# Performance work log

Measured on AMD Instinct MI355X. Metric: run time of the kernel, lower is better.

## Reference

```python
import jax, jax.numpy as jnp
import numpy as np

B, S, E, P, H, F = 4, 4096, 256, 32, 8, 1024
DH = E // H
LN_EPS = 1e-5


def setup_inputs() -> dict:
    key = jax.random.key(0)
    ks = jax.random.split(key, 12)
    dt = jnp.float32
    return {
        "src": jax.random.normal(ks[0], (B, S, E), dt),
        "pos_embed": jax.random.normal(ks[1], (B, P, S), dt),
        # learnable positional transform (pos_linear: P -> P)
        "Wpos": jax.random.normal(ks[2], (P, P), dt) * (1.0 / np.sqrt(P)),
        "bpos": jnp.zeros((P,), dt),
        # RBF kernel hyperparameters (ScaleKernel(RBFKernel)) -- positive scalars
        "lengthscale": jnp.full((), 2.0, dt),
        "outputscale": jnp.full((), 1.0, dt),
        # value / output projections of multihead attention
        "Wv": jax.random.normal(ks[3], (E, E), dt) * (1.0 / np.sqrt(E)),
        "bv": jnp.zeros((E,), dt),
        "Wo": jax.random.normal(ks[4], (E, E), dt) * (1.0 / np.sqrt(E)),
        "bo": jnp.zeros((E,), dt),
        # feed-forward
        "W1": jax.random.normal(ks[5], (F, E), dt) * (1.0 / np.sqrt(E)),
        "b1": jnp.zeros((F,), dt),
        "W2": jax.random.normal(ks[6], (E, F), dt) * (1.0 / np.sqrt(F)),
        "b2": jnp.zeros((E,), dt),
        # layer norms
        "ln1_g": jnp.ones((E,), dt), "ln1_b": jnp.zeros((E,), dt),
        "ln2_g": jnp.ones((E,), dt), "ln2_b": jnp.zeros((E,), dt),
    }


def _layer_norm(x, g, b):
    mu = jnp.mean(x, -1, keepdims=True)
    var = jnp.mean(jnp.square(x - mu), -1, keepdims=True)
    return (x - mu) * jax.lax.rsqrt(var + LN_EPS) * g + b


def _rbf_scores(x, lengthscale, outputscale):
    # x: [B, S, P] -> scaled RBF kernel matrix [B, S, S]
    xs = x / lengthscale
    sq = jnp.sum(xs * xs, axis=-1)  # [B, S]
    d2 = sq[:, :, None] + sq[:, None, :] - 2.0 * jnp.einsum('bsp,btp->bst', xs, xs)
    d2 = jnp.maximum(d2, 0.0)
    return outputscale * jnp.exp(-0.5 * d2)


def reference(src, pos_embed, Wpos, bpos, lengthscale, outputscale,
              Wv, bv, Wo, bo, W1, b1, W2, b2, ln1_g, ln1_b, ln2_g, ln2_b):
    b, s, e = src.shape
    # learnable positional transform: [B,P,S] -> [B,S,P] -> linear -> back
    pe = jnp.einsum('bps,op->bos', pos_embed, Wpos) + bpos[None, :, None]  # [B,P,S]
    # GP-kernel attention scores over sequence positions
    scores = _rbf_scores(pe.transpose(0, 2, 1), lengthscale, outputscale)  # [B,S,S]
    attn = jax.nn.softmax(scores, axis=-1)
    # value projection, per-head weighted sum (scores shared across heads)
    v = (src @ Wv.T + bv).reshape(b, s, H, DH)
    ctx = jnp.einsum('bqk,bkhd->bqhd', attn, v).reshape(b, s, e)
    attn_out = ctx @ Wo.T + bo
    x = _layer_norm(src + attn_out, ln1_g, ln1_b)
    ff = jax.nn.relu(x @ W1.T + b1) @ W2.T + b2
    return _layer_norm(x + ff, ln2_g, ln2_b)
```

## Files before the change

### kernel.cpp

```cpp
#include <hip/hip_runtime.h>
#include <stdint.h>

#define BN 4
#define SN 4096
#define EN 256
#define PN 32
#define FN 1024
#define BS (BN*SN)
#define PAUG 64

typedef uint16_t bf16_t;
typedef short v4s  __attribute__((ext_vector_type(4)));
typedef short v8s  __attribute__((ext_vector_type(8)));
typedef __bf16 bf16x8 __attribute__((ext_vector_type(8)));
typedef float v4f   __attribute__((ext_vector_type(4)));
typedef float v16f  __attribute__((ext_vector_type(16)));

#define MFMA16(a,b,c) __builtin_amdgcn_mfma_f32_16x16x32_bf16(a,b,c,0,0,0)
#define MFMA32(a,b,c) __builtin_amdgcn_mfma_f32_32x32x16_bf16(a,b,c,0,0,0)

__device__ __forceinline__ float b2f(bf16_t x){
    uint32_t u = ((uint32_t)x) << 16; float f; __builtin_memcpy(&f, &u, 4); return f;
}
__device__ __forceinline__ bf16_t f2b(float f){
    uint32_t u; __builtin_memcpy(&u, &f, 4);
    u += 0x7FFFu + ((u >> 16) & 1u);
    return (bf16_t)(u >> 16);
}
__device__ __forceinline__ bf16x8 ldb8(const bf16_t* p){
    v8s r = *(const v8s*)p; return __builtin_bit_cast(bf16x8, r);
}
__device__ __forceinline__ bf16x8 ldb8u(const bf16_t* p){
    v4s lo = *(const v4s*)p;
    v4s hi = *(const v4s*)(p + 4);
    v8s r = __builtin_shufflevector(lo, hi, 0,1,2,3,4,5,6,7);
    return __builtin_bit_cast(bf16x8, r);
}
__device__ __forceinline__ float ldsc(const float* p){ return *p; }
__device__ __forceinline__ float ldsc(const bf16_t* p){ return b2f(*p); }
__device__ __forceinline__ void stsc(float* p, float v){ *p = v; }
__device__ __forceinline__ void stsc(bf16_t* p, float v){ *p = f2b(v); }

#if __has_builtin(__builtin_amdgcn_exp2f)
__device__ __forceinline__ float fexp2(float x){ return __builtin_amdgcn_exp2f(x); }
#else
__device__ __forceinline__ float fexp2(float x){ return exp2f(x); }
#endif

#if __has_builtin(__builtin_amdgcn_cvt_pk_bf16_f32)
typedef __bf16 bf16x2 __attribute__((ext_vector_type(2)));
__device__ __forceinline__ uint32_t pkbf16(float a, float b){
    bf16x2 r = __builtin_amdgcn_cvt_pk_bf16_f32(a, b);
    return __builtin_bit_cast(uint32_t, r);
}
#else
__device__ __forceinline__ uint32_t pkbf16(float a, float b){
    return (uint32_t)f2b(a) | ((uint32_t)f2b(b) << 16);
}
#endif

typedef const __attribute__((address_space(1))) uint32_t* glds_gp;
typedef __attribute__((address_space(3))) uint32_t* glds_lp;
__device__ __forceinline__ void glds16(const bf16_t* g, bf16_t* l){
    __builtin_amdgcn_global_load_lds((glds_gp)g, (glds_lp)l, 16, 0, 0);
}

__global__ __launch_bounds__(256) void prep_kernel(
    const float* __restrict__ src, bf16_t* __restrict__ srcb,
    const float* __restrict__ Wv, bf16_t* __restrict__ Wvb,
    const float* __restrict__ Wo, bf16_t* __restrict__ Wob,
    const float* __restrict__ W1, bf16_t* __restrict__ W1b,
    const float* __restrict__ W2, bf16_t* __restrict__ W2b,
    const float* __restrict__ pos, const float* __restrict__ Wp,
    const float* __restrict__ bp,  const float* __restrict__ lsp,
    bf16_t* __restrict__ xk, bf16_t* __restrict__ xq)
{
    __shared__ float Wsh[PN*PN];
    __shared__ float bsh[PN];
    int bid = blockIdx.x;
    int tid = threadIdx.x;

    if (bid < 4736){
        const float* sp; bf16_t* dp; int off;
        if (bid < 4096){ sp = src; dp = srcb; off = (bid*256 + tid)*4; }
        else {
            int i = ((bid - 4096)*256 + tid)*4;
            if      (i <  65536){ sp=Wv; dp=Wvb; off=i; }
            else if (i < 131072){ sp=Wo; dp=Wob; off=i- 65536; }
            else if (i < 393216){ sp=W1; dp=W1b; off=i-131072; }
            else                { sp=W2; dp=W2b; off=i-393216; }
        }
        float4 f = *(const float4*)(sp + off);
        v4s o;
        o.x = (short)f2b(f.x); o.y = (short)f2b(f.y);
        o.z = (short)f2b(f.z); o.w = (short)f2b(f.w);
        *(v4s*)(dp + off) = o;
        return;
    }

    int pb = bid - 4736;
    int b  = pb >> 4;
    int s  = (pb & 15)*256 + tid;

    for (int i = tid; i < PN*PN; i += 256) Wsh[i] = Wp[i];
    if (tid < PN) bsh[tid] = bp[tid];
    __syncthreads();

    float inv_ls = 1.0f / lsp[0];
    const float c1f = 1.4426950408889634f;

    float col[PN];
    #pragma unroll
    for (int p = 0; p < PN; p++) col[p] = pos[((size_t)b*PN + p)*SN + s];

    uint16_t xb[PN], qb[PN];
    float sq = 0.f;
    #pragma unroll 4
    for (int o = 0; o < PN; o++){
        float pe = bsh[o];
        #pragma unroll
        for (int p = 0; p < PN; p++) pe += col[p] * Wsh[o*PN + p];
        float pv = pe * inv_ls;
        uint16_t h = f2b(pv);
        xb[o] = h;
        qb[o] = f2b(c1f * pv);
        float xr = b2f(h);
        sq += xr * xr;
    }

    size_t base = ((size_t)b*SN + s) * PAUG;
    v8s pk[8];
    #pragma unroll
    for (int c = 0; c < 4; c++)
        #pragma unroll
        for (int j = 0; j < 8; j++) ((short*)&pk[c])[j] = (short)xb[c*8 + j];
    #pragma unroll
    for (int c = 4; c < 8; c++)
        #pragma unroll
        for (int j = 0; j < 8; j++) ((short*)&pk[c])[j] = 0;
    ((short*)&pk[4])[0] = (short)f2b(-0.5f * sq);
    ((short*)&pk[4])[1] = (short)0x3F80;
    #pragma unroll
    for (int c = 0; c < 8; c++) *(v8s*)(xk + base + c*8) = pk[c];

    #pragma unroll
    for (int c = 0; c < 4; c++)
        #pragma unroll
        for (int j = 0; j < 8; j++) ((short*)&pk[c])[j] = (short)qb[c*8 + j];
    ((short*)&pk[4])[0] = (short)f2b(c1f);
    ((short*)&pk[4])[1] = (short)f2b(-0.5f * sq * c1f);
    #pragma unroll
    for (int c = 0; c < 8; c++) *(v8s*)(xq + base + c*8) = pk[c];
}

template<int EPI, typename OutT>
__global__ __launch_bounds__(256) void gemm_t(
    const bf16_t* __restrict__ A, const bf16_t* __restrict__ W,
    const float* __restrict__ bias, OutT* __restrict__ out,
    bf16_t* __restrict__ vt, int N, int K)
{
    __shared__ __align__(16) bf16_t At[2][4096];
    __shared__ __align__(16) bf16_t Wt[2][4096];
    int tid = threadIdx.x;
    int lane = tid & 63, wv = tid >> 6, col = lane & 15, quad = lane >> 4;
    int m0 = blockIdx.x * 64, n0 = blockIdx.y * 64;
    int nck = K >> 6;

    int srow = tid >> 3;
    int spc  = (tid & 7) ^ (srow & 7);
    const bf16_t* asrc = A + (size_t)(m0 + srow)*K + spc*8;
    const bf16_t* wsrc = W + (size_t)(n0 + srow)*K + spc*8;

    v4f acc[4];
    #pragma unroll
    for (int t = 0; t < 4; t++) acc[t] = (v4f){0.f,0.f,0.f,0.f};

    glds16(asrc, &At[0][tid*8]);
    glds16(asrc + (size_t)32*K, &At[0][2048 + tid*8]);
    glds16(wsrc, &Wt[0][tid*8]);
    glds16(wsrc + (size_t)32*K, &Wt[0][2048 + tid*8]);
    __syncthreads();

    for (int c = 0; c < nck; c++){
        int cb = c & 1;
        if (c + 1 < nck){
            glds16(asrc + (c+1)*64, &At[cb^1][tid*8]);
            glds16(asrc + (size_t)32*K + (c+1)*64, &At[cb^1][2048 + tid*8]);
            glds16(wsrc + (c+1)*64, &Wt[cb^1][tid*8]);
            glds16(wsrc + (size_t)32*K + (c+1)*64, &Wt[cb^1][2048 + tid*8]);
        }
        #pragma unroll
        for (int kc = 0; kc < 2; kc++){
            int pc = ((kc*4 + quad) ^ (col & 7)) * 8;
            bf16x8 a = ldb8(&At[cb][(wv*16 + col)*64 + pc]);
            #pragma unroll
            for (int t = 0; t < 4; t++){
                bf16x8 b = ldb8(&Wt[cb][(t*16 + col)*64 + pc]);
                acc[t] = MFMA16(a, b, acc[t]);
            }
        }
        __syncthreads();
    }

    float bfv[4];
    #pragma unroll
    for (int t = 0; t < 4; t++) bfv[t] = bias[n0 + t*16 + col];

    if constexpr (EPI == 3){
        __shared__ uint16_t Tsh[64*74];
        #pragma unroll
        for (int r = 0; r < 4; r++)
            #pragma unroll
            for (int t = 0; t < 4; t++)
                Tsh[(wv*16 + quad*4 + r)*74 + t*16 + col] = f2b(acc[t][r] + bfv[t]);
        __syncthreads();
        int e = tid >> 2, sc = tid & 3;
        int b = m0 >> 12;
        int sbat = m0 & (SN-1);
        int eb   = (n0 + e) >> 5;
        int l31e = (n0 + e) & 31;
        int k16  = (sbat >> 4) + sc;
        v8s p0, p1;
        #pragma unroll
        for (int i = 0; i < 8; i++) ((short*)&p0)[i] = (short)Tsh[(sc*16 + i)*74 + e];
        #pragma unroll
        for (int i = 0; i < 8; i++) ((short*)&p1)[i] = (short)Tsh[(sc*16 + 8 + i)*74 + e];
        bf16_t* dst = vt + ((((size_t)b*8 + eb)*256 + k16)*64 + l31e)*8;
        *(v8s*)dst = p0;
        *(v8s*)(dst + 256) = p1;
    } else {
        #pragma unroll
        for (int r = 0; r < 4; r++){
            int row = m0 + wv*16 + quad*4 + r;
            #pragma unroll
            for (int t = 0; t < 4; t++){
                float y = acc[t][r] + bfv[t];
                if constexpr (EPI == 1) y = fmaxf(y, 0.f);
                stsc(out + (size_t)row*N + n0 + t*16 + col, y);
            }
        }
    }
}

template<int EPI>
__global__ __launch_bounds__(256, 2) void gemm128(
    const bf16_t* __restrict__ A, const bf16_t* __restrict__ W,
    const float* __restrict__ bias, bf16_t* __restrict__ out,
    int N, int K)
{
    __shared__ __align__(16) bf16_t At[2][8192];
    __shared__ __align__(16) bf16_t Wt[2][8192];
    int tid = threadIdx.x;
    int lane = tid & 63, wv = tid >> 6, col = lane & 15, quad = lane >> 4;
    int m0 = blockIdx.x * 128, n0 = blockIdx.y * 128;
    int nck = K >> 6;

    int srow = tid >> 3;
    int spc  = (tid & 7) ^ (srow & 7);
    const bf16_t* asrc = A + (size_t)(m0 + srow)*K + spc*8;
    const bf16_t* wsrc = W + (size_t)(n0 + srow)*K + spc*8;

    v4f acc[2][8];
    #pragma unroll
    for (int mi = 0; mi < 2; mi++)
        #pragma unroll
        for (int t = 0; t < 8; t++) acc[mi][t] = (v4f){0.f,0.f,0.f,0.f};

    #pragma unroll
    for (int s = 0; s < 4; s++){
        glds16(asrc + (size_t)(s*32)*K, &At[0][s*2048 + tid*8]);
        glds16(wsrc + (size_t)(s*32)*K, &Wt[0][s*2048 + tid*8]);
    }
    __syncthreads();

    for (int c = 0; c < nck; c++){
        int cb = c & 1;
        if (c + 1 < nck){
            #pragma unroll
            for (int s = 0; s < 4; s++){
                glds16(asrc + (size_t)(s*32)*K + (c+1)*64, &At[cb^1][s*2048 + tid*8]);
                glds16(wsrc + (size_t)(s*32)*K + (c+1)*64, &Wt[cb^1][s*2048 + tid*8]);
            }
        }
        #pragma unroll
        for (int kc = 0; kc < 2; kc++){
            int pc = ((kc*4 + quad) ^ (col & 7)) * 8;
            bf16x8 a[2];
            #pragma unroll
            for (int mi = 0; mi < 2; mi++)
                a[mi] = ldb8(&At[cb][(wv*32 + mi*16 + col)*64 + pc]);
            #pragma unroll
            for (int t = 0; t < 8; t++){
                bf16x8 b = ldb8(&Wt[cb][(t*16 + col)*64 + pc]);
                #pragma unroll
                for (int mi = 0; mi < 2; mi++)
                    acc[mi][t] = MFMA16(a[mi], b, acc[mi][t]);
            }
        }
        __syncthreads();
    }

    float bfv[8];
    #pragma unroll
    for (int t = 0; t < 8; t++) bfv[t] = bias[n0 + t*16 + col];

    #pragma unroll
    for (int mi = 0; mi < 2; mi++){
        #pragma unroll
        for (int r = 0; r < 4; r++){
            int row = m0 + wv*32 + mi*16 + quad*4 + r;
            #pragma unroll
            for (int t = 0; t < 8; t++){
                float y = acc[mi][t][r] + bfv[t];
                if constexpr (EPI == 1) y = fmaxf(y, 0.f);
                out[(size_t)row*N + n0 + t*16 + col] = f2b(y);
            }
        }
    }
}

template<typename OutT, typename ResT>
__global__ __launch_bounds__(256) void ln_kernel(
    const bf16_t* __restrict__ y, const ResT* __restrict__ res,
    const float* __restrict__ gamma, const float* __restrict__ beta,
    OutT* __restrict__ out)
{
    int tid = threadIdx.x;
    int row = blockIdx.x * 32 + (tid >> 3);
    int l8  = tid & 7;
    size_t base = (size_t)row * EN;
    float v[32];
    float s1 = 0.f, s2 = 0.f;
    #pragma unroll
    for (int i = 0; i < 4; i++){
        int off = l8*8 + i*64;
        v8s a = *(const v8s*)(y + base + off);
        #pragma unroll
        for (int j = 0; j < 8; j++){
            float t = b2f((bf16_t)(uint16_t)a[j]) + ldsc(res + base + off + j);
            v[i*8 + j] = t; s1 += t; s2 += t*t;
        }
    }
    #pragma unroll
    for (int m = 1; m <= 4; m <<= 1){
        s1 += __shfl_xor(s1, m);
        s2 += __shfl_xor(s2, m);
    }
    float mu = s1 * (1.f/256.f);
    float rs = rsqrtf(s2 * (1.f/256.f) - mu*mu + 1e-5f);
    #pragma unroll
    for (int i = 0; i < 4; i++){
        int off = l8*8 + i*64;
        #pragma unroll
        for (int j = 0; j < 8; j++)
            stsc(out + base + off + j, (v[i*8+j]-mu)*rs*gamma[off+j] + beta[off+j]);
    }
}

__global__ __launch_bounds__(512, 4) void attn_kernel(
    const bf16_t* __restrict__ xk, const bf16_t* __restrict__ xq,
    const bf16_t* __restrict__ vf, const float* __restrict__ osp,
    bf16_t* __restrict__ ctx)
{
    __shared__ __align__(16) bf16_t Wtb[2][64*132];
    __shared__ __align__(16) bf16_t Qs[64*64];
    __shared__ float densh[8][64];
    __shared__ float dent[64];

    int tid  = threadIdx.x;
    int lane = tid & 63;
    int wv   = tid >> 6;
    int col  = lane & 15;
    int quad = lane >> 4;
    int l31  = lane & 31;
    int half = lane >> 5;

    int bid = blockIdx.x;
    int b   = (bid & 7) >> 1;
    int qi  = ((bid >> 3) << 1) | (bid & 1);
    int q0  = qi * 64;

    float k2 = 1.4426950408889634f * osp[0];

    const bf16_t* xkb = xk + (size_t)b * SN * PAUG;
    const bf16_t* xqb = xq + (size_t)b * SN * PAUG;
    const bf16_t* vfb = vf + (((size_t)b*8 + wv)*256)*512 + lane*8;

    {
        int qrow = tid >> 3;
        int qpc  = (tid & 7) ^ (qrow & 7);
        glds16(xqb + (size_t)(q0 + qrow)*PAUG + qpc*8, &Qs[tid*8]);
    }

    v16f acc[2];
    #pragma unroll
    for (int qg = 0; qg < 2; qg++)
        #pragma unroll
        for (int i = 0; i < 16; i++) acc[qg][i] = 0.f;
    float den[4] = {0.f, 0.f, 0.f, 0.f};
    const v4f zero = (v4f){0.f,0.f,0.f,0.f};

    bf16x8 kf0, kf1;
    {
        const bf16_t* kr = xkb + (size_t)(wv*16 + col)*PAUG + quad*8;
        kf0 = ldb8(kr); kf1 = ldb8(kr + 32);
    }

    __syncthreads();

    for (int c = 0; c < 32; c++){
        int cb = c & 1;
        bf16x8 vr[8];
        #pragma unroll
        for (int sk = 0; sk < 8; sk++)
            vr[sk] = ldb8(vfb + (size_t)(c*8 + sk)*512);

        #pragma unroll
        for (int qg = 0; qg < 2; qg++){
            #pragma unroll
            for (int g2 = 0; g2 < 2; g2++){
                int qr = qg*32 + g2*16 + col;
                bf16x8 qa = ldb8(&Qs[qr*64 + ((quad    ) ^ (col & 7))*8]);
                bf16x8 qb = ldb8(&Qs[qr*64 + ((4 + quad) ^ (col & 7))*8]);
                v4f st = MFMA16(kf0, qa, zero);
                st = MFMA16(kf1, qb, st);
                #pragma unroll
                for (int rp = 0; rp < 2; rp++){
                    float w0 = fexp2(fmaf(k2, fexp2(st[rp*2+0]), -k2));
                    float w1 = fexp2(fmaf(k2, fexp2(st[rp*2+1]), -k2));
                    den[qg*2+g2] += w0 + w1;
                    *(uint32_t*)&Wtb[cb][qr*132 + wv*16 + quad*4 + rp*2]
                        = pkbf16(w0, w1);
                }
            }
        }

        if (c + 1 < 32){
            const bf16_t* kr = xkb + (size_t)((c+1)*128 + wv*16 + col)*PAUG + quad*8;
            kf0 = ldb8(kr); kf1 = ldb8(kr + 32);
        }

        asm volatile("s_waitcnt lgkmcnt(0)" ::: "memory");
        __builtin_amdgcn_s_barrier();
        __builtin_amdgcn_sched_barrier(0);

        #pragma unroll
        for (int qg = 0; qg < 2; qg++){
            #pragma unroll
            for (int sk4 = 0; sk4 < 2; sk4++){
                bf16x8 af[4];
                #pragma unroll
                for (int j = 0; j < 4; j++)
                    af[j] = ldb8u(&Wtb[cb][(qg*32 + l31)*132 + (sk4*4 + j)*16 + half*8]);
                #pragma unroll
                for (int j = 0; j < 4; j++)
                    acc[qg] = MFMA32(af[j], vr[sk4*4 + j], acc[qg]);
            }
        }
    }

    #pragma unroll
    for (int d = 0; d < 4; d++){
        den[d] += __shfl_xor(den[d], 16);
        den[d] += __shfl_xor(den[d], 32);
    }
    if (lane < 16){
        #pragma unroll
        for (int qg = 0; qg < 2; qg++)
            #pragma unroll
            for (int g2 = 0; g2 < 2; g2++)
                densh[wv][qg*32 + g2*16 + lane] = den[qg*2+g2];
    }
    __syncthreads();
    if (tid < 64){
        float s = 0.f;
        #pragma unroll
        for (int w = 0; w < 8; w++) s += densh[w][tid];
        dent[tid] = 1.f / s;
    }
    __syncthreads();

    size_t obase = ((size_t)b*SN + q0) * EN + wv*32;
    #pragma unroll
    for (int qg = 0; qg < 2; qg++){
        #pragma unroll
        for (int rg = 0; rg < 16; rg++){
            int row = (rg & 3) + 8*(rg >> 2) + 4*half;
            float inv = dent[qg*32 + row];
            ctx[obase + (size_t)(qg*32 + row)*EN + l31] = f2b(acc[qg][rg] * inv);
        }
    }
}

extern "C" void kernel_launch(void* const* d_in, const int* in_sizes, int n_in,
                              void* d_out, int out_size, void* d_ws, size_t ws_size,
                              hipStream_t stream)
{
    (void)in_sizes; (void)n_in; (void)out_size; (void)ws_size;
    const float* src  = (const float*)d_in[0];
    const float* pos  = (const float*)d_in[1];
    const float* Wpos = (const float*)d_in[2];
    const float* bpos = (const float*)d_in[3];
    const float* ls   = (const float*)d_in[4];
    const float* os   = (const float*)d_in[5];
    const float* Wv   = (const float*)d_in[6];
    const float* bv   = (const float*)d_in[7];
    const float* Wo   = (const float*)d_in[8];
    const float* bo   = (const float*)d_in[9];
    const float* W1   = (const float*)d_in[10];
    const float* b1   = (const float*)d_in[11];
    const float* W2   = (const float*)d_in[12];
    const float* b2   = (const float*)d_in[13];
    const float* g1   = (const float*)d_in[14];
    const float* be1  = (const float*)d_in[15];
    const float* g2   = (const float*)d_in[16];
    const float* be2  = (const float*)d_in[17];

    char* w = (char*)d_ws;
    bf16_t* xkb  = (bf16_t*)(w);
    bf16_t* xqb  = (bf16_t*)(w + ( 2u<<20));
    bf16_t* Wvb  = (bf16_t*)(w + ( 4u<<20));
    bf16_t* Wob  = (bf16_t*)(w + ( 4u<<20) + (1u<<18));
    bf16_t* W1b  = (bf16_t*)(w + ( 5u<<20));
    bf16_t* W2b  = (bf16_t*)(w + ( 6u<<20));
    bf16_t* srcb = (bf16_t*)(w + ( 8u<<20));
    bf16_t* y2   = (bf16_t*)(w + ( 8u<<20));
    bf16_t* vtg  = (bf16_t*)(w + (16u<<20));
    bf16_t* y1   = (bf16_t*)(w + (16u<<20));
    bf16_t* ctx  = (bf16_t*)(w + (24u<<20));
    bf16_t* xws  = (bf16_t*)(w + (24u<<20));
    bf16_t* hws  = (bf16_t*)(w + (32u<<20));

    prep_kernel<<<dim3(4800), 256, 0, stream>>>(
        src, srcb, Wv, Wvb, Wo, Wob, W1, W1b, W2, W2b,
        pos, Wpos, bpos, ls, xkb, xqb);

    gemm_t<3, bf16_t><<<dim3(BS/64, EN/64), 256, 0, stream>>>(
        srcb, Wvb, bv, (bf16_t*)nullptr, vtg, EN, EN);
    attn_kernel<<<dim3(256), 512, 0, stream>>>(xkb, xqb, vtg, os, ctx);
    gemm128<0><<<dim3(BS/128, EN/128), 256, 0, stream>>>(
        ctx, Wob, bo, y1, EN, EN);
    ln_kernel<bf16_t, bf16_t><<<dim3(BS/32), 256, 0, stream>>>(y1, srcb, g1, be1, xws);
    gemm128<1><<<dim3(BS/128, FN/128), 256, 0, stream>>>(
        xws, W1b, b1, hws, FN, EN);
    gemm128<0><<<dim3(BS/128, EN/128), 256, 0, stream>>>(
        hws, W2b, b2, y2, EN, FN);
    ln_kernel<float, bf16_t><<<dim3(BS/32), 256, 0, stream>>>(y2, xws, g2, be2, (float*)d_out);
}
```

Measured before the change: 248.9 us.

## Fuse output and FFN-down GEMMs with residual add and LayerNorm

Adds a gemm_ln kernel in which each 512-thread block computes a full 32x256 row tile, then adds bias and the residual and performs LayerNorm. Row statistics are reduced across waves through shared memory. It replaces the separate gemm128 and ln_kernel pairs after attention and after the FFN, removing the bf16 intermediate round trips and two launches. The cost is that every block re-streams the whole weight matrix with a narrow M tile, so more traffic goes through L2 and the small tile reuses data less than the 128x128 GEMM did.

```diff
diff --git a/kernel.cpp b/kernel.cpp
--- a/kernel.cpp
+++ b/kernel.cpp
@@ -319,41 +319,114 @@
     }
 }
 
-template<typename OutT, typename ResT>
-__global__ __launch_bounds__(256) void ln_kernel(
-    const bf16_t* __restrict__ y, const ResT* __restrict__ res,
+template<typename OutT>
+__global__ __launch_bounds__(512, 4) void gemm_ln(
+    const bf16_t* __restrict__ A, const bf16_t* __restrict__ W,
+    const float* __restrict__ bias, const bf16_t* __restrict__ res,
     const float* __restrict__ gamma, const float* __restrict__ beta,
-    OutT* __restrict__ out)
+    OutT* __restrict__ out, int K)
 {
+    __shared__ __align__(16) bf16_t At[2][32*64];
+    __shared__ __align__(16) bf16_t Wt[2][256*64];
+    __shared__ float lnb[4][32][2];
+
     int tid = threadIdx.x;
-    int row = blockIdx.x * 32 + (tid >> 3);
-    int l8  = tid & 7;
-    size_t base = (size_t)row * EN;
-    float v[32];
-    float s1 = 0.f, s2 = 0.f;
-    #pragma unroll
-    for (int i = 0; i < 4; i++){
-        int off = l8*8 + i*64;
-        v8s a = *(const v8s*)(y + base + off);
-        #pragma unroll
-        for (int j = 0; j < 8; j++){
-            float t = b2f((bf16_t)(uint16_t)a[j]) + ldsc(res + base + off + j);
-            v[i*8 + j] = t; s1 += t; s2 += t*t;
-        }
-    }
-    #pragma unroll
-    for (int m = 1; m <= 4; m <<= 1){
-        s1 += __shfl_xor(s1, m);
-        s2 += __shfl_xor(s2, m);
-    }
-    float mu = s1 * (1.f/256.f);
-    float rs = rsqrtf(s2 * (1.f/256.f) - mu*mu + 1e-5f);
-    #pragma unroll
-    for (int i = 0; i < 4; i++){
-        int off = l8*8 + i*64;
-        #pragma unroll
-        for (int j = 0; j < 8; j++)
-            stsc(out + base + off + j, (v[i*8+j]-mu)*rs*gamma[off+j] + beta[off+j]);
+    int lane = tid & 63, wv = tid >> 6, col = lane & 15, quad = lane >> 4;
+    int mw = wv >> 2;
+    int nw = wv & 3;
+    int m0 = blockIdx.x * 32;
+    int nck = K >> 6;
+
+    int arow = (tid & 255) >> 3;
+    int apc  = (tid & 7) ^ (arow & 7);
+    const bf16_t* asrc = A + (size_t)(m0 + arow)*K + apc*8;
+    int wr0  = tid >> 3;
+    const bf16_t* wsrc[4];
+    #pragma unroll
+    for (int s = 0; s < 4; s++){
+        int wrow = s*64 + wr0;
+        int wpc  = (tid & 7) ^ (wrow & 7);
+        wsrc[s] = W + (size_t)wrow*K + wpc*8;
+    }
+
+    v4f acc[4];
+    #pragma unroll
+    for (int t = 0; t < 4; t++) acc[t] = (v4f){0.f,0.f,0.f,0.f};
+
+    if (tid < 256) glds16(asrc, &At[0][tid*8]);
+    #pragma unroll
+    for (int s = 0; s < 4; s++) glds16(wsrc[s], &Wt[0][s*4096 + tid*8]);
+    __syncthreads();
+
+    for (int c = 0; c < nck; c++){
+        int cb = c & 1;
+        if (c + 1 < nck){
+            if (tid < 256) glds16(asrc + (c+1)*64, &At[cb^1][tid*8]);
+            #pragma unroll
+            for (int s = 0; s < 4; s++)
+                glds16(wsrc[s] + (c+1)*64, &Wt[cb^1][s*4096 + tid*8]);
+        }
+        #pragma unroll
+        for (int kc = 0; kc < 2; kc++){
+            int pc = ((kc*4 + quad) ^ (col & 7)) * 8;
+            bf16x8 a = ldb8(&At[cb][(mw*16 + col)*64 + pc]);
+            #pragma unroll
+            for (int t = 0; t < 4; t++){
+                bf16x8 b = ldb8(&Wt[cb][(nw*64 + t*16 + col)*64 + pc]);
+                acc[t] = MFMA16(a, b, acc[t]);
+            }
+        }
+        __syncthreads();
+    }
+
+    float bfv[4];
+    #pragma unroll
+    for (int t = 0; t < 4; t++) bfv[t] = bias[nw*64 + t*16 + col];
+
+    float v[4][4];
+    float s1[4], s2[4];
+    #pragma unroll
+    for (int r = 0; r < 4; r++){ s1[r] = 0.f; s2[r] = 0.f; }
+    #pragma unroll
+    for (int r = 0; r < 4; r++){
+        int row = m0 + mw*16 + quad*4 + r;
+        #pragma unroll
+        for (int t = 0; t < 4; t++){
+            float x = acc[t][r] + bfv[t]
+                    + b2f(res[(size_t)row*EN + nw*64 + t*16 + col]);
+            v[t][r] = x; s1[r] += x; s2[r] += x*x;
+        }
+    }
+    #pragma unroll
+    for (int r = 0; r < 4; r++){
+        #pragma unroll
+        for (int m = 1; m <= 8; m <<= 1){
+            s1[r] += __shfl_xor(s1[r], m);
+            s2[r] += __shfl_xor(s2[r], m);
+        }
+    }
+    if (col == 0){
+        #pragma unroll
+        for (int r = 0; r < 4; r++){
+            int rl = mw*16 + quad*4 + r;
+            lnb[nw][rl][0] = s1[r];
+            lnb[nw][rl][1] = s2[r];
+        }
+    }
+    __syncthreads();
+    #pragma unroll
+    for (int r = 0; r < 4; r++){
+        int rl  = mw*16 + quad*4 + r;
+        int row = m0 + rl;
+        float S1 = lnb[0][rl][0] + lnb[1][rl][0] + lnb[2][rl][0] + lnb[3][rl][0];
+        float S2 = lnb[0][rl][1] + lnb[1][rl][1] + lnb[2][rl][1] + lnb[3][rl][1];
+        float mu = S1 * (1.f/256.f);
+        float rs = rsqrtf(S2 * (1.f/256.f) - mu*mu + 1e-5f);
+        #pragma unroll
+        for (int t = 0; t < 4; t++){
+            int gi = nw*64 + t*16 + col;
+            stsc(out + (size_t)row*EN + gi, (v[t][r]-mu)*rs*gamma[gi] + beta[gi]);
+        }
     }
 }
 
@@ -524,9 +597,7 @@
     bf16_t* W1b  = (bf16_t*)(w + ( 5u<<20));
     bf16_t* W2b  = (bf16_t*)(w + ( 6u<<20));
     bf16_t* srcb = (bf16_t*)(w + ( 8u<<20));
-    bf16_t* y2   = (bf16_t*)(w + ( 8u<<20));
     bf16_t* vtg  = (bf16_t*)(w + (16u<<20));
-    bf16_t* y1   = (bf16_t*)(w + (16u<<20));
     bf16_t* ctx  = (bf16_t*)(w + (24u<<20));
     bf16_t* xws  = (bf16_t*)(w + (24u<<20));
     bf16_t* hws  = (bf16_t*)(w + (32u<<20));
@@ -538,12 +609,10 @@
     gemm_t<3, bf16_t><<<dim3(BS/64, EN/64), 256, 0, stream>>>(
         srcb, Wvb, bv, (bf16_t*)nullptr, vtg, EN, EN);
     attn_kernel<<<dim3(256), 512, 0, stream>>>(xkb, xqb, vtg, os, ctx);
-    gemm128<0><<<dim3(BS/128, EN/128), 256, 0, stream>>>(
-        ctx, Wob, bo, y1, EN, EN);
-    ln_kernel<bf16_t, bf16_t><<<dim3(BS/32), 256, 0, stream>>>(y1, srcb, g1, be1, xws);
+    gemm_ln<bf16_t><<<dim3(BS/32), 512, 0, stream>>>(
+        ctx, Wob, bo, srcb, g1, be1, xws, EN);
     gemm128<1><<<dim3(BS/128, FN/128), 256, 0, stream>>>(
         xws, W1b, b1, hws, FN, EN);
-    gemm128<0><<<dim3(BS/128, EN/128), 256, 0, stream>>>(
-        hws, W2b, b2, y2, EN, FN);
-    ln_kernel<float, bf16_t><<<dim3(BS/32), 256, 0, stream>>>(y2, xws, g2, be2, (float*)d_out);
-}
+    gemm_ln<float><<<dim3(BS/32), 512, 0, stream>>>(
+        hws, W2b, b2, xws, g2, be2, (float*)d_out, FN);
+}
```

Result: faster. 232.5 us (-6.6%).
